# Performance work log

Measured on AMD Instinct MI355X. Metric: run time of the kernel, lower is better.

Reference implementation:

```python
import jax, jax.numpy as jnp
import numpy as np

D_MODEL = 1024
N_HEADS = 16
DEPTH = D_MODEL // N_HEADS


def setup_inputs() -> dict:
    key = jax.random.key(0)
    ks = jax.random.split(key, 11)
    B, S = 2, 2048
    scale = 1.0 / np.sqrt(D_MODEL)
    inp = {
        "Q": jax.random.normal(ks[0], (B, S, D_MODEL), dtype=jnp.float32),
        "K": jax.random.normal(ks[1], (B, S, D_MODEL), dtype=jnp.float32),
        "V": jax.random.normal(ks[2], (B, S, D_MODEL), dtype=jnp.float32),
        "Wq": jax.random.normal(ks[3], (D_MODEL, D_MODEL), dtype=jnp.float32) * scale,
        "bq": jnp.zeros((D_MODEL,), dtype=jnp.float32),
        "Wk": jax.random.normal(ks[4], (D_MODEL, D_MODEL), dtype=jnp.float32) * scale,
        "bk": jnp.zeros((D_MODEL,), dtype=jnp.float32),
        "Wv": jax.random.normal(ks[5], (D_MODEL, D_MODEL), dtype=jnp.float32) * scale,
        "bv": jnp.zeros((D_MODEL,), dtype=jnp.float32),
        "Wo": jax.random.normal(ks[6], (D_MODEL, D_MODEL), dtype=jnp.float32) * scale,
        "bo": jnp.zeros((D_MODEL,), dtype=jnp.float32),
    }
    return inp


def reference(Q, K, V, Wq, bq, Wk, bk, Wv, bv, Wo, bo):
    B, S, _ = Q.shape
    # Linear projections (torch Linear: x @ W.T + b)
    q = Q @ Wq.T + bq
    k = K @ Wk.T + bk
    v = V @ Wv.T + bv
    # split heads: [B, S, H, depth] -> [B, H, S, depth]
    q = q.reshape(B, S, N_HEADS, DEPTH).transpose(0, 2, 1, 3)
    k = k.reshape(B, S, N_HEADS, DEPTH).transpose(0, 2, 1, 3)
    v = v.reshape(B, S, N_HEADS, DEPTH).transpose(0, 2, 1, 3)
    # scaled dot-product attention, full [B,H,S,S] scores as in the original
    scores = jnp.einsum("bhqd,bhkd->bhqk", q, k) / jnp.sqrt(jnp.float32(DEPTH))
    attn = jax.nn.softmax(scores, axis=-1)
    out = jnp.einsum("bhqk,bhkd->bhqd", attn, v)
    # combine heads
    out = out.transpose(0, 2, 1, 3).reshape(B, S, D_MODEL)
    return out @ Wo.T + bo
```

## Files before the change

kernel.cpp:

```cpp
#include <hip/hip_runtime.h>


typedef unsigned short u16;
typedef unsigned int   u32;
typedef __attribute__((ext_vector_type(8)))  __bf16 bf16x8;
typedef __attribute__((ext_vector_type(8)))  u16    u16x8;
typedef __attribute__((ext_vector_type(4)))  u32    u32x4;
typedef __attribute__((ext_vector_type(4)))  float  f32x4;
typedef __attribute__((ext_vector_type(16))) float  f32x16;

#define MFMA16(a,b,c) __builtin_amdgcn_mfma_f32_16x16x32_bf16((a),(b),(c),0,0,0)
#define MFMA32(a,b,c) __builtin_amdgcn_mfma_f32_32x32x16_bf16((a),(b),(c),0,0,0)

__device__ __forceinline__ u16 f2bf(float f) {
    unsigned int u = __float_as_uint(f);
    return (u16)((u + 0x7FFF + ((u >> 16) & 1)) >> 16);
}
__device__ __forceinline__ u32 cvtpk(float a, float b) {
    u32 d;
    asm("v_cvt_pk_bf16_f32 %0, %1, %2" : "=v"(d) : "v"(a), "v"(b));
    return d;
}
__device__ __forceinline__ void gl2lds16(const void* g, void* l) {
    __builtin_amdgcn_global_load_lds((const __attribute__((address_space(1))) unsigned int*)g,
                                     (__attribute__((address_space(3))) unsigned int*)l, 16, 0, 0);
}

__global__ __launch_bounds__(256)
void cvt_all(const float* __restrict__ Q, const float* __restrict__ K, const float* __restrict__ V,
             const float* __restrict__ W0, const float* __restrict__ W1,
             const float* __restrict__ W2, const float* __restrict__ W3,
             u16* __restrict__ oq, u16* __restrict__ ok, u16* __restrict__ ov,
             u16* __restrict__ o0, u16* __restrict__ o1, u16* __restrict__ o2, u16* __restrict__ o3)
{
    const int bx = blockIdx.x;
    const float* s; u16* d; int local;
    if (bx < 6144) {
        int t = bx >> 11; local = bx & 2047;
        s = (t == 0) ? Q : (t == 1) ? K : V;
        d = (t == 0) ? oq : (t == 1) ? ok : ov;
    } else {
        int t = (bx - 6144) >> 9; local = (bx - 6144) & 511;
        s = (t == 0) ? W0 : (t == 1) ? W1 : (t == 2) ? W2 : W3;
        d = (t == 0) ? o0 : (t == 1) ? o1 : (t == 2) ? o2 : o3;
    }
    size_t i = ((size_t)local * 256 + threadIdx.x) * 8;
    f32x4 lo = *(const f32x4*)(s + i), hi = *(const f32x4*)(s + i + 4);
    u16x8 v;
    #pragma unroll
    for (int t = 0; t < 4; t++) { v[t] = f2bf(lo[t]); v[4 + t] = f2bf(hi[t]); }
    *(u16x8*)(d + i) = v;
}

template<int LAYOUT, int TM>
__device__ __forceinline__ void gemm_body64(const u16* __restrict__ A, const u16* __restrict__ W,
                                            const float* __restrict__ bias, void* __restrict__ outv,
                                            u16* S, int m0, int n0, float scale)
{
    constexpr int MI = TM / 32;
    u16* As = S;
    u16* Bs = S + TM * 64;
    const int tid  = threadIdx.x;
    const int wave = tid >> 6, lane = tid & 63;
    const int quad = lane >> 4, l16 = lane & 15;
    const int wr = (wave >> 1) * (TM / 2), wc = (wave & 1) * 64;
    const int s7 = l16 & 7;

    f32x4 acc[MI][4] = {};

    for (int k0 = 0; k0 < 1024; k0 += 64) {
        __syncthreads();
        #pragma unroll
        for (int t = 0; t < MI; t++) {
            int idx = t * 256 + tid;
            int r = idx >> 3, c = idx & 7;
            gl2lds16(A + (size_t)(m0 + r) * 1024 + k0 + ((c ^ (r & 7)) * 8), As + idx * 8);
        }
        #pragma unroll
        for (int t = 0; t < 4; t++) {
            int idx = t * 256 + tid;
            int r = idx >> 3, c = idx & 7;
            gl2lds16(W + (size_t)(n0 + r) * 1024 + k0 + ((c ^ (r & 7)) * 8), Bs + idx * 8);
        }
        __syncthreads();
        #pragma unroll
        for (int ks = 0; ks < 2; ks++) {
            const int sw = (ks * 4 + quad) ^ s7;
            bf16x8 af[MI], bfr[4];
            #pragma unroll
            for (int i = 0; i < MI; i++)
                af[i] = *(const bf16x8*)(As + (wr + i * 16 + l16) * 64 + sw * 8);
            #pragma unroll
            for (int j = 0; j < 4; j++)
                bfr[j] = *(const bf16x8*)(Bs + (wc + j * 16 + l16) * 64 + sw * 8);
            #pragma unroll
            for (int i = 0; i < MI; i++)
                #pragma unroll
                for (int j = 0; j < 4; j++)
                    acc[i][j] = MFMA16(af[i], bfr[j], acc[i][j]);
        }
    }

    if (LAYOUT == 2) {
        float bv[4];
        #pragma unroll
        for (int j = 0; j < 4; j++) bv[j] = bias[n0 + wc + j * 16 + l16];
        #pragma unroll
        for (int i = 0; i < MI; i++)
            #pragma unroll
            for (int j = 0; j < 4; j++) {
                int gn = n0 + wc + j * 16 + l16;
                #pragma unroll
                for (int r = 0; r < 4; r++) {
                    int gm = m0 + wr + i * 16 + quad * 4 + r;
                    ((float*)outv)[(size_t)gm * 1024 + gn] = acc[i][j][r] + bv[j];
                }
            }
    } else {
        float bv[4], bm[MI][4];
        if (LAYOUT == 0) {
            #pragma unroll
            for (int j = 0; j < 4; j++) bv[j] = bias[n0 + wc + j * 16 + l16];
        } else {
            #pragma unroll
            for (int i = 0; i < MI; i++)
                #pragma unroll
                for (int r = 0; r < 4; r++) bm[i][r] = bias[m0 + wr + i * 16 + quad * 4 + r];
        }
        __syncthreads();
        u16* WR = S + wave * (16 * 68);
        #pragma unroll
        for (int i = 0; i < MI; i++) {
            #pragma unroll
            for (int j = 0; j < 4; j++)
                #pragma unroll
                for (int r = 0; r < 4; r++) {
                    float v = (acc[i][j][r] + (LAYOUT == 0 ? bv[j] : bm[i][r])) * scale;
                    WR[(quad * 4 + r) * 68 + j * 16 + l16] = f2bf(v);
                }
            int gm0 = m0 + wr + i * 16, gn0 = n0 + wc;
            size_t gb;
            if (LAYOUT == 0) gb = (((size_t)(gm0 >> 11) * 16 + (gn0 >> 6)) * 2048 + (gm0 & 2047)) * 64;
            else             gb = (((size_t)(gn0 >> 11) * 16 + (gm0 >> 6)) * 64 + (gm0 & 63)) * 2048 + (gn0 & 2047);
            #pragma unroll
            for (int st = 0; st < 2; st++) {
                int chunk = st * 64 + lane;
                int row = chunk >> 3, c8 = chunk & 7;
                u16x8 v = *(const u16x8*)(WR + row * 68 + c8 * 8);
                size_t ga = (LAYOUT == 0) ? gb + row * 64 + c8 * 8 : gb + (size_t)row * 2048 + c8 * 8;
                *(u16x8*)((u16*)outv + ga) = v;
            }
        }
    }
}

#define CST 0.18033688011112042f

__global__ __launch_bounds__(256, 3)
void gemm_qkv(const u16* __restrict__ Qb, const u16* __restrict__ Kb, const u16* __restrict__ Vb,
              const u16* __restrict__ Wq, const u16* __restrict__ Wk, const u16* __restrict__ Wv,
              const float* __restrict__ bq, const float* __restrict__ bk, const float* __restrict__ bv,
              u16* __restrict__ qh, u16* __restrict__ kh, u16* __restrict__ vt)
{
    __shared__ __align__(16) u16 S[128 * 64 * 2];
    const int z = blockIdx.z;
    if (z < 2) {
        gemm_body64<0, 128>(z == 0 ? Qb : Kb, z == 0 ? Wq : Wk, z == 0 ? bq : bk,
                            z == 0 ? qh : kh, S, blockIdx.y * 128, blockIdx.x * 128,
                            z == 0 ? CST : 1.0f);
    } else {
        gemm_body64<3, 128>(Wv, Vb, bv, vt, S, blockIdx.x * 128, blockIdx.y * 128, 1.0f);
    }
}

__global__ __launch_bounds__(256, 2)
void gemm_o(const u16* __restrict__ A, const u16* __restrict__ W,
            const float* __restrict__ bias, float* __restrict__ out)
{
    __shared__ __align__(16) u16 S[64 * 64 + 128 * 64];
    gemm_body64<2, 64>(A, W, bias, out, S, blockIdx.y * 64, blockIdx.x * 128, 1.0f);
}

__global__ __launch_bounds__(256, 2)
void attn_fused(const u16* __restrict__ qh, const u16* __restrict__ kh,
                const u16* __restrict__ vt, u16* __restrict__ out)
{
    __shared__ __align__(16) u16 Ks[256 * 64];
    __shared__ __align__(16) u16 Vs[64 * 256];

    const int tid  = threadIdx.x;
    const int wave = tid >> 6, lane = tid & 63;
    const int l31 = lane & 31, h = lane >> 5;

    const int lid = blockIdx.x + 16 * (blockIdx.y + 16 * blockIdx.z);
    const int w   = (lid & 7) * 64 + (lid >> 3);
    const int q0  = (w & 15) * 128;
    const int hh  = (w >> 4) & 15, b = w >> 8;

    const size_t head = (size_t)(b * 16 + hh);
    const u16* qh_h = qh + head * (2048 * 64);
    const u16* kh_h = kh + head * (2048 * 64);
    const u16* vt_h = vt + head * (64 * 2048);

    bf16x8 qf[4];
    #pragma unroll
    for (int ks = 0; ks < 4; ks++)
        qf[ks] = *(const bf16x8*)(qh_h + (size_t)(q0 + wave * 32 + l31) * 64 + ks * 16 + h * 8);

    const u32 one2 = 0x3F803F80u;
    const u32x4 onesw = {one2, one2, one2, one2};
    const bf16x8 onesf = __builtin_bit_cast(bf16x8, onesw);

    f32x16 oacc[2] = {};
    f32x16 lacc = {};

    for (int kt = 0; kt < 8; kt++) {
        const int kv0 = kt * 256;
        __syncthreads();
        #pragma unroll
        for (int it = 0; it < 8; it++) {
            int idx = it * 256 + tid;
            int kr = idx >> 3, kc = idx & 7;
            gl2lds16(kh_h + (size_t)(kv0 + kr) * 64 + ((kc ^ (kr & 7)) * 8), Ks + idx * 8);
            int vr = idx >> 5, vc = idx & 31;
            gl2lds16(vt_h + (size_t)vr * 2048 + kv0 + ((vc ^ (vr & 15)) * 8), Vs + idx * 8);
        }
        __syncthreads();

        #pragma unroll
        for (int mt = 0; mt < 8; mt++) {
            f32x16 sacc = {};
            #pragma unroll
            for (int ks = 0; ks < 4; ks++) {
                int row = mt * 32 + l31;
                bf16x8 kf = *(const bf16x8*)(Ks + row * 64 + (((ks * 2 + h) ^ (l31 & 7)) * 8));
                sacc = MFMA32(kf, qf[ks], sacc);
            }
            u32 P[4][2];
            #pragma unroll
            for (int g = 0; g < 4; g++) {
                P[g][0] = cvtpk(__builtin_amdgcn_exp2f(sacc[g * 4 + 0]),
                                __builtin_amdgcn_exp2f(sacc[g * 4 + 1]));
                P[g][1] = cvtpk(__builtin_amdgcn_exp2f(sacc[g * 4 + 2]),
                                __builtin_amdgcn_exp2f(sacc[g * 4 + 3]));
            }
            #pragma unroll
            for (int c16 = 0; c16 < 2; c16++) {
                u32 x0 = P[2 * c16][0], y0 = P[2 * c16 + 1][0];
                u32 x1 = P[2 * c16][1], y1 = P[2 * c16 + 1][1];
                asm volatile("v_permlane32_swap_b32 %0, %1" : "+v"(x0), "+v"(y0));
                asm volatile("v_permlane32_swap_b32 %0, %1" : "+v"(x1), "+v"(y1));
                u32x4 bw = {x0, x1, y0, y1};
                bf16x8 pB = __builtin_bit_cast(bf16x8, bw);
                lacc = MFMA32(onesf, pB, lacc);
                int c = mt * 4 + c16 * 2 + h;
                #pragma unroll
                for (int dt = 0; dt < 2; dt++) {
                    int d = dt * 32 + l31;
                    bf16x8 vf = *(const bf16x8*)(Vs + d * 256 + ((c ^ (l31 & 15)) * 8));
                    oacc[dt] = MFMA32(vf, pB, oacc[dt]);
                }
            }
        }
    }

    float inv = 1.0f / lacc[0];

    size_t ob = ((size_t)(b * 2048 + q0 + wave * 32 + l31)) * 1024 + hh * 64;
    #pragma unroll
    for (int dt = 0; dt < 2; dt++)
        #pragma unroll
        for (int g = 0; g < 4; g++) {
            int d0 = dt * 32 + 8 * g + 4 * h;
            *(u32*)((u16*)out + ob + d0)     = cvtpk(oacc[dt][g * 4 + 0] * inv, oacc[dt][g * 4 + 1] * inv);
            *(u32*)((u16*)out + ob + d0 + 2) = cvtpk(oacc[dt][g * 4 + 2] * inv, oacc[dt][g * 4 + 3] * inv);
        }
}

extern "C" void kernel_launch(void* const* d_in, const int* in_sizes, int n_in,
                              void* d_out, int out_size, void* d_ws, size_t ws_size,
                              hipStream_t stream)
{
    const float* Q   = (const float*)d_in[0];
    const float* Kin = (const float*)d_in[1];
    const float* V   = (const float*)d_in[2];
    const float* Wq  = (const float*)d_in[3];
    const float* bq  = (const float*)d_in[4];
    const float* Wk  = (const float*)d_in[5];
    const float* bk  = (const float*)d_in[6];
    const float* Wv  = (const float*)d_in[7];
    const float* bv  = (const float*)d_in[8];
    const float* Wo  = (const float*)d_in[9];
    const float* bo  = (const float*)d_in[10];

    const size_t TS = (size_t)2 * 2048 * 1024;
    const size_t WS = (size_t)1024 * 1024;
    u16* Qb  = (u16*)d_ws;
    u16* Kb  = Qb + TS;
    u16* Vb  = Kb + TS;
    u16* qh  = Vb + TS;
    u16* kh  = qh + TS;
    u16* vt  = kh + TS;
    u16* Wqb = vt + TS;
    u16* Wkb = Wqb + WS;
    u16* Wvb = Wkb + WS;
    u16* Wob = Wvb + WS;
    u16* at  = Qb;

    cvt_all<<<dim3(8192), 256, 0, stream>>>(Q, Kin, V, Wq, Wk, Wv, Wo,
                                            Qb, Kb, Vb, Wqb, Wkb, Wvb, Wob);
    gemm_qkv<<<dim3(8, 32, 3), 256, 0, stream>>>(Qb, Kb, Vb, Wqb, Wkb, Wvb, bq, bk, bv, qh, kh, vt);
    attn_fused<<<dim3(16, 16, 2), 256, 0, stream>>>(qh, kh, vt, at);
    gemm_o<<<dim3(8, 64), 256, 0, stream>>>(at, Wob, bo, (float*)d_out);
}
```

Baseline: 211.7 us.

## Fuse fp32-to-bf16 conversion into GEMM tile staging, drop separate convert pass

Removes the standalone conversion kernel that wrote bf16 copies of the inputs and weights. The GEMM kernels now load fp32 tiles directly, pack them to bf16 in registers and store them into shared memory. This saves a full read/write pass over about 64MB of inputs plus one launch. In exchange, the GEMMs read twice the bytes per tile reload and lose the asynchronous global-to-LDS copy path for fp32 operands.

```diff
diff --git a/kernel.cpp b/kernel.cpp
--- a/kernel.cpp
+++ b/kernel.cpp
@@ -25,35 +25,15 @@
     __builtin_amdgcn_global_load_lds((const __attribute__((address_space(1))) unsigned int*)g,
                                      (__attribute__((address_space(3))) unsigned int*)l, 16, 0, 0);
 }
-
-__global__ __launch_bounds__(256)
-void cvt_all(const float* __restrict__ Q, const float* __restrict__ K, const float* __restrict__ V,
-             const float* __restrict__ W0, const float* __restrict__ W1,
-             const float* __restrict__ W2, const float* __restrict__ W3,
-             u16* __restrict__ oq, u16* __restrict__ ok, u16* __restrict__ ov,
-             u16* __restrict__ o0, u16* __restrict__ o1, u16* __restrict__ o2, u16* __restrict__ o3)
-{
-    const int bx = blockIdx.x;
-    const float* s; u16* d; int local;
-    if (bx < 6144) {
-        int t = bx >> 11; local = bx & 2047;
-        s = (t == 0) ? Q : (t == 1) ? K : V;
-        d = (t == 0) ? oq : (t == 1) ? ok : ov;
-    } else {
-        int t = (bx - 6144) >> 9; local = (bx - 6144) & 511;
-        s = (t == 0) ? W0 : (t == 1) ? W1 : (t == 2) ? W2 : W3;
-        d = (t == 0) ? o0 : (t == 1) ? o1 : (t == 2) ? o2 : o3;
-    }
-    size_t i = ((size_t)local * 256 + threadIdx.x) * 8;
-    f32x4 lo = *(const f32x4*)(s + i), hi = *(const f32x4*)(s + i + 4);
-    u16x8 v;
-    #pragma unroll
-    for (int t = 0; t < 4; t++) { v[t] = f2bf(lo[t]); v[4 + t] = f2bf(hi[t]); }
-    *(u16x8*)(d + i) = v;
-}
-
-template<int LAYOUT, int TM>
-__device__ __forceinline__ void gemm_body64(const u16* __restrict__ A, const u16* __restrict__ W,
+__device__ __forceinline__ void stage_f32_chunk(const float* __restrict__ g, u16* l) {
+    f32x4 lo = *(const f32x4*)g, hi = *(const f32x4*)(g + 4);
+    u32x4 w = { cvtpk(lo[0], lo[1]), cvtpk(lo[2], lo[3]),
+                cvtpk(hi[0], hi[1]), cvtpk(hi[2], hi[3]) };
+    *(u32x4*)l = w;
+}
+
+template<int LAYOUT, int TM, int AF32, int BF32>
+__device__ __forceinline__ void gemm_body64(const void* __restrict__ Av, const void* __restrict__ Wv,
                                             const float* __restrict__ bias, void* __restrict__ outv,
                                             u16* S, int m0, int n0, float scale)
 {
@@ -74,13 +54,17 @@
         for (int t = 0; t < MI; t++) {
             int idx = t * 256 + tid;
             int r = idx >> 3, c = idx & 7;
-            gl2lds16(A + (size_t)(m0 + r) * 1024 + k0 + ((c ^ (r & 7)) * 8), As + idx * 8);
+            size_t off = (size_t)(m0 + r) * 1024 + k0 + ((c ^ (r & 7)) * 8);
+            if constexpr (AF32) stage_f32_chunk((const float*)Av + off, As + idx * 8);
+            else                gl2lds16((const u16*)Av + off, As + idx * 8);
         }
         #pragma unroll
         for (int t = 0; t < 4; t++) {
             int idx = t * 256 + tid;
             int r = idx >> 3, c = idx & 7;
-            gl2lds16(W + (size_t)(n0 + r) * 1024 + k0 + ((c ^ (r & 7)) * 8), Bs + idx * 8);
+            size_t off = (size_t)(n0 + r) * 1024 + k0 + ((c ^ (r & 7)) * 8);
+            if constexpr (BF32) stage_f32_chunk((const float*)Wv + off, Bs + idx * 8);
+            else                gl2lds16((const u16*)Wv + off, Bs + idx * 8);
         }
         __syncthreads();
         #pragma unroll
@@ -157,28 +141,28 @@
 #define CST 0.18033688011112042f
 
 __global__ __launch_bounds__(256, 3)
-void gemm_qkv(const u16* __restrict__ Qb, const u16* __restrict__ Kb, const u16* __restrict__ Vb,
-              const u16* __restrict__ Wq, const u16* __restrict__ Wk, const u16* __restrict__ Wv,
+void gemm_qkv(const float* __restrict__ Q, const float* __restrict__ Kin, const float* __restrict__ V,
+              const float* __restrict__ Wq, const float* __restrict__ Wk, const float* __restrict__ Wv,
               const float* __restrict__ bq, const float* __restrict__ bk, const float* __restrict__ bv,
               u16* __restrict__ qh, u16* __restrict__ kh, u16* __restrict__ vt)
 {
     __shared__ __align__(16) u16 S[128 * 64 * 2];
     const int z = blockIdx.z;
     if (z < 2) {
-        gemm_body64<0, 128>(z == 0 ? Qb : Kb, z == 0 ? Wq : Wk, z == 0 ? bq : bk,
-                            z == 0 ? qh : kh, S, blockIdx.y * 128, blockIdx.x * 128,
-                            z == 0 ? CST : 1.0f);
+        gemm_body64<0, 128, 1, 1>(z == 0 ? Q : Kin, z == 0 ? Wq : Wk, z == 0 ? bq : bk,
+                                  z == 0 ? qh : kh, S, blockIdx.y * 128, blockIdx.x * 128,
+                                  z == 0 ? CST : 1.0f);
     } else {
-        gemm_body64<3, 128>(Wv, Vb, bv, vt, S, blockIdx.x * 128, blockIdx.y * 128, 1.0f);
+        gemm_body64<3, 128, 1, 1>(Wv, V, bv, vt, S, blockIdx.x * 128, blockIdx.y * 128, 1.0f);
     }
 }
 
 __global__ __launch_bounds__(256, 2)
-void gemm_o(const u16* __restrict__ A, const u16* __restrict__ W,
+void gemm_o(const u16* __restrict__ A, const float* __restrict__ W,
             const float* __restrict__ bias, float* __restrict__ out)
 {
     __shared__ __align__(16) u16 S[64 * 64 + 128 * 64];
-    gemm_body64<2, 64>(A, W, bias, out, S, blockIdx.y * 64, blockIdx.x * 128, 1.0f);
+    gemm_body64<2, 64, 0, 1>(A, W, bias, out, S, blockIdx.y * 64, blockIdx.x * 128, 1.0f);
 }
 
 __global__ __launch_bounds__(256, 2)
@@ -294,22 +278,12 @@
     const float* bo  = (const float*)d_in[10];
 
     const size_t TS = (size_t)2 * 2048 * 1024;
-    const size_t WS = (size_t)1024 * 1024;
-    u16* Qb  = (u16*)d_ws;
-    u16* Kb  = Qb + TS;
-    u16* Vb  = Kb + TS;
-    u16* qh  = Vb + TS;
-    u16* kh  = qh + TS;
-    u16* vt  = kh + TS;
-    u16* Wqb = vt + TS;
-    u16* Wkb = Wqb + WS;
-    u16* Wvb = Wkb + WS;
-    u16* Wob = Wvb + WS;
-    u16* at  = Qb;
-
-    cvt_all<<<dim3(8192), 256, 0, stream>>>(Q, Kin, V, Wq, Wk, Wv, Wo,
-                                            Qb, Kb, Vb, Wqb, Wkb, Wvb, Wob);
-    gemm_qkv<<<dim3(8, 32, 3), 256, 0, stream>>>(Qb, Kb, Vb, Wqb, Wkb, Wvb, bq, bk, bv, qh, kh, vt);
+    u16* qh = (u16*)d_ws;
+    u16* kh = qh + TS;
+    u16* vt = kh + TS;
+    u16* at = vt + TS;
+
+    gemm_qkv<<<dim3(8, 32, 3), 256, 0, stream>>>(Q, Kin, V, Wq, Wk, Wv, bq, bk, bv, qh, kh, vt);
     attn_fused<<<dim3(16, 16, 2), 256, 0, stream>>>(qh, kh, vt, at);
-    gemm_o<<<dim3(8, 64), 256, 0, stream>>>(at, Wob, bo, (float*)d_out);
-}
+    gemm_o<<<dim3(8, 64), 256, 0, stream>>>(at, Wo, bo, (float*)d_out);
+}
```

Measured after the change: 243.4 us. 14.9% more time.
